# Performance work log

Hardware: AMD Instinct MI355X
Metric: run time of the kernel (lower is better)

The kernel has to match this reference:

```python
import jax, jax.numpy as jnp
import numpy as np

B, S, E, H = 2, 2048, 1024, 16
HD = E // H
SCALE = 1.0 / np.sqrt(HD)
PR_QKV = 0.05   # precision_ratio for q/k/v (critical_attention=False)
PR_OUT = 0.10
ROUTE_THR = 0.05  # gradient_threshold (critical_attention=False)
LN_EPS = 1e-5


def rpb_linear(x, W, b, precision_ratio):
    """ResidualPrecisionBoostLinear: ternary-quantized weight (threshold 0.7*mean|W|,
    per-tensor scale) plus top-`precision_ratio` fraction of residual kept full precision."""
    absW = jnp.abs(W)
    thr = 0.7 * jnp.mean(absW)
    tmask = (absW > thr).astype(W.dtype)
    scale = jnp.sum(absW * tmask) / jnp.maximum(jnp.sum(tmask), 1.0)
    Wq = scale * jnp.sign(W) * tmask
    res = W - Wq
    k = int(precision_ratio * W.size)
    kth = jax.lax.top_k(jnp.abs(res).ravel(), k)[0][-1]
    W_eff = Wq + res * (jnp.abs(res) >= kth).astype(W.dtype)
    return x @ W_eff.T + b


def selective_route(x, threshold):
    # forward: zero out small-magnitude activations (straight-through in training)
    return x * (jnp.abs(x) >= threshold).astype(x.dtype)


def layer_norm(x, g, b):
    mu = jnp.mean(x, axis=-1, keepdims=True)
    var = jnp.mean(jnp.square(x - mu), axis=-1, keepdims=True)
    return (x - mu) * jax.lax.rsqrt(var + LN_EPS) * g + b


def setup_inputs() -> dict:
    key = jax.random.key(0)
    ks = jax.random.split(key, 12)
    f = lambda k, shp, s=1.0: jax.random.normal(k, shp, dtype=jnp.float32) * s
    return {
        "query": f(ks[0], (B, S, E)),
        "key": f(ks[1], (B, S, E)),
        "value": f(ks[2], (B, S, E)),
        "Wq": f(ks[3], (E, E), 0.02), "bq": jnp.zeros((E,), jnp.float32),
        "Wk": f(ks[4], (E, E), 0.02), "bk": jnp.zeros((E,), jnp.float32),
        "Wv": f(ks[5], (E, E), 0.02), "bv": jnp.zeros((E,), jnp.float32),
        "Wo": f(ks[6], (E, E), 0.02), "bo": jnp.zeros((E,), jnp.float32),
        "ln_g": jnp.ones((E,), jnp.float32),
        "ln_b": jnp.zeros((E,), jnp.float32),
    }


def reference(query, key, value, Wq, bq, Wk, bk, Wv, bv, Wo, bo, ln_g, ln_b):
    qn = layer_norm(query, ln_g, ln_b)
    q = selective_route(rpb_linear(qn, Wq, bq, PR_QKV), ROUTE_THR)
    k = selective_route(rpb_linear(key, Wk, bk, PR_QKV), ROUTE_THR)
    v = selective_route(rpb_linear(value, Wv, bv, PR_QKV), ROUTE_THR)
    # [B,S,E] -> [B,H,S,HD]
    q = q.reshape(B, S, H, HD).transpose(0, 2, 1, 3)
    k = k.reshape(B, S, H, HD).transpose(0, 2, 1, 3)
    v = v.reshape(B, S, H, HD).transpose(0, 2, 1, 3)
    scores = jnp.einsum("bhqd,bhkd->bhqk", q, k) * SCALE
    attn = jax.nn.softmax(scores, axis=-1)   # dropout is identity in eval
    ctx = jnp.einsum("bhqk,bhkd->bhqd", attn, v)
    ctx = ctx.transpose(0, 2, 1, 3).reshape(B, S, E)
    return rpb_linear(ctx, Wo, bo, PR_OUT)
```

## Files before the change

kernel.cpp:

```cpp
#include <hip/hip_runtime.h>
#include <stdio.h>
#include <stdint.h>

#define BB 2
#define SS 2048
#define ED 1024
#define HH 16
#define HDD 64
#define MROWS 4096
#define NW_ELEM 1048576u

typedef unsigned short ushortT;
typedef __attribute__((ext_vector_type(8))) short bf16x8;
typedef __attribute__((ext_vector_type(4))) float f32x4;
typedef __attribute__((ext_vector_type(16))) float f32x16;

#define U_WHI 0u
#define U_WLO 4194304u
#define U_XQ  8388608u
#define U_XK  12582912u
#define U_XV  16777216u
#define U_QH  20971520u
#define U_KH  25165824u
#define U_VH  29360128u
#define LP_OFF  33554432u
#define P0_OFF  67108864u
#define P1_OFF  83886080u
#define SMALL_OFF  100663296u
#define HIST_OFF   SMALL_OFF
#define ABS_OFF    (SMALL_OFF + 16384u)
#define MSK_OFF    (ABS_OFF + 32u)
#define CNT_OFF    (MSK_OFF + 32u)
#define SMALL_BYTES 16464u
#define WS_NEEDED  (SMALL_OFF + SMALL_BYTES)

#define SC44 17592186044416.0f
#define INV44 (1.0 / 17592186044416.0)
#define QSCALE 0.18033688011112042f

__device__ __forceinline__ const float* wsel(int w, const float* W0, const float* W1,
                                             const float* W2, const float* W3) {
  return w == 0 ? W0 : w == 1 ? W1 : w == 2 ? W2 : W3;
}

__device__ __forceinline__ ushortT f2bf(float x) {
  unsigned u = __float_as_uint(x);
  unsigned r = (u + 0x7FFFu + ((u >> 16) & 1u)) >> 16;
  return (ushortT)r;
}
__device__ __forceinline__ float bf2f(ushortT b) {
  return __uint_as_float(((unsigned)b) << 16);
}
__device__ __forceinline__ void bsplit(float x, ushortT& h, ushortT& l) {
  ushortT hb = f2bf(x);
  float hf = bf2f(hb);
  h = hb;
  l = f2bf(x - hf);
}
__device__ __forceinline__ unsigned pkbf(float a, float b) {
  unsigned r;
  asm("v_cvt_pk_bf16_f32 %0, %1, %2" : "=v"(r) : "v"(a), "v"(b));
  return r;
}
__device__ __forceinline__ void plswap(unsigned& a, unsigned& b) {
  asm("v_permlane32_swap_b32 %0, %1" : "+v"(a), "+v"(b));
}

__device__ __forceinline__ void gld_lds16(const ushortT* g, ushortT* s) {
  __builtin_amdgcn_global_load_lds((__attribute__((address_space(1))) void*)g,
                                   (__attribute__((address_space(3))) void*)s, 16, 0, 0);
}

__device__ __forceinline__ float get_thr(const unsigned long long* sAbs, int w) {
  return 0.7f * (float)((double)sAbs[w] * INV44 / 1048576.0);
}
__device__ __forceinline__ float get_scale(const unsigned long long* sMsk,
                                           const unsigned* cnt, int w) {
  double s = (double)sMsk[w] * INV44;
  return (float)s / fmaxf((float)cnt[w], 1.0f);
}

__device__ __forceinline__ void scan_sel(const unsigned* hist, unsigned& k, unsigned& prefix,
                                         unsigned* sh, int t) {
  sh[t] = hist[t];
  __syncthreads();
  for (int off = 1; off < 256; off <<= 1) {
    unsigned add = (t + off < 256) ? sh[t + off] : 0u;
    __syncthreads();
    sh[t] += add;
    __syncthreads();
  }
  int sel = __syncthreads_count((int)(sh[t] >= k)) - 1;
  unsigned suf = sh[sel];
  k -= (suf - hist[sel]);
  prefix = (prefix << 8) | (unsigned)sel;
  __syncthreads();
}

__global__ __launch_bounds__(256) void k_wstats(const float* W0, const float* W1,
                                                const float* W2, const float* W3,
                                                unsigned long long* sAbs) {
  const int w = blockIdx.y, t = threadIdx.x;
  const float* W = wsel(w, W0, W1, W2, W3) + blockIdx.x * 4096;
  unsigned long long s = 0;
#pragma unroll
  for (int r = 0; r < 4; r++) {
    float4 v = *(const float4*)(W + (t + 256 * r) * 4);
    s += (unsigned long long)(fabsf(v.x) * SC44);
    s += (unsigned long long)(fabsf(v.y) * SC44);
    s += (unsigned long long)(fabsf(v.z) * SC44);
    s += (unsigned long long)(fabsf(v.w) * SC44);
  }
  __shared__ unsigned long long sd[256];
  sd[t] = s;
  __syncthreads();
  for (int off = 128; off > 0; off >>= 1) {
    if (t < off) sd[t] += sd[t + off];
    __syncthreads();
  }
  if (!t) atomicAdd(&sAbs[w], sd[0]);
}

__global__ __launch_bounds__(256) void k_masked(const float* W0, const float* W1,
                                                const float* W2, const float* W3,
                                                const unsigned long long* sAbs,
                                                unsigned long long* sMsk, unsigned* sCnt) {
  const int w = blockIdx.y, t = threadIdx.x;
  const float thr = get_thr(sAbs, w);
  const float* W = wsel(w, W0, W1, W2, W3) + blockIdx.x * 4096;
  unsigned long long s = 0;
  unsigned c = 0;
#pragma unroll
  for (int r = 0; r < 4; r++) {
    float4 v = *(const float4*)(W + (t + 256 * r) * 4);
    float xs[4] = {v.x, v.y, v.z, v.w};
#pragma unroll
    for (int q = 0; q < 4; q++) {
      float a = fabsf(xs[q]);
      if (a > thr) { s += (unsigned long long)(a * SC44); c++; }
    }
  }
  __shared__ unsigned long long sd[256];
  __shared__ unsigned sc[256];
  sd[t] = s; sc[t] = c;
  __syncthreads();
  for (int off = 128; off > 0; off >>= 1) {
    if (t < off) { sd[t] += sd[t + off]; sc[t] += sc[t + off]; }
    __syncthreads();
  }
  if (!t) { atomicAdd(&sMsk[w], sd[0]); atomicAdd(&sCnt[w], sc[0]); }
}

__global__ __launch_bounds__(256) void k_hist(const float* W0, const float* W1,
                                              const float* W2, const float* W3,
                                              const unsigned long long* sAbs,
                                              const unsigned long long* sMsk,
                                              const unsigned* sCnt,
                                              unsigned* histG, int pass) {
  const int w = blockIdx.y, t = threadIdx.x;
  __shared__ unsigned sh[256];
  __shared__ unsigned h[256];
  const float thr = get_thr(sAbs, w);
  const float scale = get_scale(sMsk, sCnt, w);
  unsigned k = (w == 3) ? 104857u : 52428u, prefix = 0u;
  for (int pp = 0; pp < pass; pp++)
    scan_sel(histG + (pp * 4 + w) * 256, k, prefix, sh, t);

  h[t] = 0;
  __syncthreads();
  const float* W = wsel(w, W0, W1, W2, W3) + blockIdx.x * 4096;
  const int shift1 = 32 - 8 * pass;
  const int shift2 = 24 - 8 * pass;
#pragma unroll
  for (int r = 0; r < 4; r++) {
    float4 v = *(const float4*)(W + (t + 256 * r) * 4);
    float xs[4] = {v.x, v.y, v.z, v.w};
#pragma unroll
    for (int q = 0; q < 4; q++) {
      float x = xs[q];
      float a = fabsf(x);
      float wq = (a > thr) ? copysignf(scale, x) : 0.0f;
      unsigned bits = __float_as_uint(fabsf(x - wq));
      if (pass == 0) {
        atomicAdd(&h[bits >> 24], 1u);
      } else {
        if ((bits >> shift1) == prefix)
          atomicAdd(&h[(bits >> shift2) & 255u], 1u);
      }
    }
  }
  __syncthreads();
  if (h[t]) atomicAdd(&histG[(pass * 4 + w) * 256 + t], h[t]);
}

__global__ __launch_bounds__(256) void k_weff(const float* W0, const float* W1,
                                              const float* W2, const float* W3,
                                              const unsigned long long* sAbs,
                                              const unsigned long long* sMsk,
                                              const unsigned* sCnt,
                                              const unsigned* histG,
                                              ushortT* Whi, ushortT* Wlo) {
  const int w = blockIdx.y, t = threadIdx.x;
  __shared__ unsigned sh[256];
  const float thr = get_thr(sAbs, w);
  const float scale = get_scale(sMsk, sCnt, w);
  unsigned k = (w == 3) ? 104857u : 52428u, kth = 0u;
  for (int pp = 0; pp < 4; pp++)
    scan_sel(histG + (pp * 4 + w) * 256, k, kth, sh, t);

  const unsigned idx = (blockIdx.x * 256 + t) * 4;
  const float* W = wsel(w, W0, W1, W2, W3);
  float4 v = *(const float4*)(W + idx);
  float xs[4] = {v.x, v.y, v.z, v.w};
  ushort4 h4, l4;
#pragma unroll
  for (int c = 0; c < 4; c++) {
    float x = xs[c];
    float a = fabsf(x);
    float wq = (a > thr) ? copysignf(scale, x) : 0.0f;
    float res = x - wq;
    unsigned bits = __float_as_uint(fabsf(res));
    float we = wq + ((bits >= kth) ? res : 0.0f);
    ushortT hh, ll;
    bsplit(we, hh, ll);
    ((ushortT*)&h4)[c] = hh;
    ((ushortT*)&l4)[c] = ll;
  }
  *(ushort4*)&Whi[(size_t)w * NW_ELEM + idx] = h4;
  *(ushort4*)&Wlo[(size_t)w * NW_ELEM + idx] = l4;
}

__global__ __launch_bounds__(256) void k_pre(const float* __restrict__ query,
                                             const float* __restrict__ key,
                                             const float* __restrict__ value,
                                             const float* __restrict__ g,
                                             const float* __restrict__ b,
                                             ushortT* __restrict__ Xq,
                                             ushortT* __restrict__ Xk,
                                             ushortT* __restrict__ Xv) {
  const int t = threadIdx.x;
  if (blockIdx.y == 0) {
    const int row = blockIdx.x;
    __shared__ float red[8];
    float4 v = *(const float4*)&query[(size_t)row * ED + t * 4];
    float s = v.x + v.y + v.z + v.w;
#pragma unroll
    for (int m = 32; m; m >>= 1) s += __shfl_xor(s, m, 64);
    if ((t & 63) == 0) red[t >> 6] = s;
    __syncthreads();
    float mu = (red[0] + red[1] + red[2] + red[3]) * (1.0f / 1024.0f);
    float dx = v.x - mu, dy = v.y - mu, dz = v.z - mu, dw = v.w - mu;
    float s2 = dx * dx + dy * dy + dz * dz + dw * dw;
#pragma unroll
    for (int m = 32; m; m >>= 1) s2 += __shfl_xor(s2, m, 64);
    if ((t & 63) == 0) red[4 + (t >> 6)] = s2;
    __syncthreads();
    float var = (red[4] + red[5] + red[6] + red[7]) * (1.0f / 1024.0f);
    float inv = rsqrtf(var + 1e-5f);
    float4 gg = *(const float4*)&g[t * 4];
    float4 bb = *(const float4*)&b[t * 4];
    float ys[4] = {dx * inv * gg.x + bb.x, dy * inv * gg.y + bb.y,
                   dz * inv * gg.z + bb.z, dw * inv * gg.w + bb.w};
    ushort4 h4;
#pragma unroll
    for (int c = 0; c < 4; c++) ((ushortT*)&h4)[c] = f2bf(ys[c]);
    *(ushort4*)&Xq[(size_t)row * ED + t * 4] = h4;
  } else {
    const float* src = (blockIdx.y == 1) ? key : value;
    ushortT* dst = (blockIdx.y == 1) ? Xk : Xv;
    const int i = (blockIdx.x * 256 + t) * 4;
    float4 v = *(const float4*)&src[i];
    ushort4 h4;
    h4.x = f2bf(v.x); h4.y = f2bf(v.y); h4.z = f2bf(v.z); h4.w = f2bf(v.w);
    *(ushort4*)&dst[i] = h4;
  }
}

__device__ __forceinline__ f32x4 mfma16(bf16x8 a, bf16x8 b, f32x4 c) {
  return __builtin_amdgcn_mfma_f32_16x16x32_bf16(a, b, c, 0, 0, 0);
}

__global__ __launch_bounds__(256, 2) void k_gemm_qkv(
    const ushortT* __restrict__ Xq, const ushortT* __restrict__ Xk,
    const ushortT* __restrict__ Xv,
    const ushortT* __restrict__ Whi, const ushortT* __restrict__ Wlo,
    const float* __restrict__ bq, const float* __restrict__ bk,
    const float* __restrict__ bv,
    ushortT* __restrict__ Qo, ushortT* __restrict__ Ko, ushortT* __restrict__ Vo) {
  __shared__ __align__(16) ushortT sAh[2 * 8192];
  __shared__ __align__(16) ushortT sBh[2 * 4096];
  __shared__ __align__(16) ushortT sBl[2 * 4096];
  const int t = threadIdx.x;
  const int w = t >> 6, l = t & 63;
  const int wr = w >> 1, wc = w & 1;

  const int which = blockIdx.x >> 9;
  const int wid = blockIdx.x & 511;
  int id2 = (wid & 7) * 64 + (wid >> 3);
  const int m0 = (id2 >> 4) * 128, n0 = (id2 & 15) * 64;

  const ushortT* A = which == 0 ? Xq : which == 1 ? Xk : Xv;
  const ushortT* Wh = Whi + (unsigned)which * NW_ELEM;
  const ushortT* Wl = Wlo + 2u * NW_ELEM;
  const float* bias = which == 0 ? bq : which == 1 ? bk : bv;
  const bool wlo = (which == 2);

  const int sr = l >> 3, sg = l & 7;
  const int swz = sg ^ sr;

  auto stage = [&](int kt, int buf) {
#pragma unroll
    for (int s2 = 0; s2 < 4; s2++) {
      int seg = w * 4 + s2;
      size_t gsrc = (size_t)(m0 + seg * 8 + sr) * ED + kt * 64 + swz * 8;
      gld_lds16(A + gsrc, sAh + buf * 8192 + seg * 512);
    }
#pragma unroll
    for (int s2 = 0; s2 < 2; s2++) {
      int seg = w * 2 + s2;
      size_t gsrc = (size_t)(n0 + seg * 8 + sr) * ED + kt * 64 + swz * 8;
      gld_lds16(Wh + gsrc, sBh + buf * 4096 + seg * 512);
      if (wlo) gld_lds16(Wl + gsrc, sBl + buf * 4096 + seg * 512);
    }
  };

  f32x4 acc[4][2];
#pragma unroll
  for (int i = 0; i < 4; i++)
#pragma unroll
    for (int j = 0; j < 2; j++) acc[i][j] = (f32x4){0.0f, 0.0f, 0.0f, 0.0f};

  auto compute = [&](int buf) {
#pragma unroll
    for (int ks = 0; ks < 2; ks++) {
      bf16x8 ah[4], bh2[2], bl2[2];
      const int G = ks * 4 + (l >> 4);
#pragma unroll
      for (int i = 0; i < 4; i++) {
        int r = wr * 64 + i * 16 + (l & 15);
        ah[i] = *(const bf16x8*)&sAh[buf * 8192 + r * 64 + ((G ^ (l & 7)) << 3)];
      }
#pragma unroll
      for (int j = 0; j < 2; j++) {
        int r = wc * 32 + j * 16 + (l & 15);
        int off = buf * 4096 + r * 64 + ((G ^ (l & 7)) << 3);
        bh2[j] = *(const bf16x8*)&sBh[off];
        if (wlo) bl2[j] = *(const bf16x8*)&sBl[off];
      }
#pragma unroll
      for (int i = 0; i < 4; i++)
#pragma unroll
        for (int j = 0; j < 2; j++) {
          acc[i][j] = mfma16(ah[i], bh2[j], acc[i][j]);
          if (wlo) acc[i][j] = mfma16(ah[i], bl2[j], acc[i][j]);
        }
    }
  };

  stage(0, 0);
  __syncthreads();
  for (int kt = 0; kt < 16; ++kt) {
    if (kt < 15) stage(kt + 1, (kt + 1) & 1);
    compute(kt & 1);
    __syncthreads();
  }

  const int coln = l & 15, row4 = (l >> 4) * 4;
  float bn[2];
#pragma unroll
  for (int j = 0; j < 2; j++) bn[j] = bias[n0 + wc * 32 + j * 16 + coln];
  const int b_ = m0 >> 11, h_ = n0 >> 6;

  if (which < 2) {
    const float osc = (which == 0) ? QSCALE : 1.0f;
    ushortT* C = (which == 0) ? Qo : Ko;
#pragma unroll
    for (int i = 0; i < 4; i++)
#pragma unroll
      for (int j = 0; j < 2; j++) {
        int hd = wc * 32 + j * 16 + coln;
#pragma unroll
        for (int r = 0; r < 4; r++) {
          int m = m0 + wr * 64 + i * 16 + row4 + r;
          int s_ = m & 2047;
          float y = acc[i][j][r] + bn[j];
          y = (fabsf(y) >= 0.05f) ? y : 0.0f;
          y *= osc;
          C[((size_t)(b_ * HH + h_) * SS + s_) * HDD + hd] = f2bf(y);
        }
      }
  } else {
#pragma unroll
    for (int i = 0; i < 4; i++)
#pragma unroll
      for (int j = 0; j < 2; j++) {
        int hd = wc * 32 + j * 16 + coln;
        int s0_ = (m0 + wr * 64 + i * 16 + row4) & 2047;
        ushort4 h4;
#pragma unroll
        for (int r = 0; r < 4; r++) {
          float y = acc[i][j][r] + bn[j];
          y = (fabsf(y) >= 0.05f) ? y : 0.0f;
          ((ushortT*)&h4)[r] = f2bf(y);
        }
        *(ushort4*)&Vo[((size_t)(b_ * HH + h_) * HDD + hd) * SS + s0_] = h4;
      }
  }
}

__global__ __launch_bounds__(256, 2) void k_gemmo(
    const ushortT* __restrict__ Ah, const ushortT* __restrict__ Al,
    const ushortT* __restrict__ Wh, const ushortT* __restrict__ Wl,
    const float* __restrict__ bias, float* __restrict__ Cf) {
  __shared__ __align__(16) ushortT sAh[2 * 4096], sAl[2 * 4096];
  __shared__ __align__(16) ushortT sBh[2 * 2048], sBl[2 * 2048];
  const int t = threadIdx.x;
  const int w = t >> 6, l = t & 63;
  const int wr = w >> 1, wc = w & 1;

  int id = blockIdx.x;
  int id2 = (id & 7) * 64 + (id >> 3);
  const int m0 = (id2 >> 4) * 128, n0 = (id2 & 15) * 64;

  const int srow = l >> 2;
  const int sgr = (l & 3) ^ ((l >> 3) & 3);

  auto stage = [&](int kt, int buf) {
    const int c0 = kt * 32 + sgr * 8;
#pragma unroll
    for (int s2 = 0; s2 < 2; s2++) {
      int seg = w * 2 + s2;
      size_t ga = (size_t)(m0 + seg * 16 + srow) * ED + c0;
      gld_lds16(Ah + ga, sAh + buf * 4096 + seg * 512);
      gld_lds16(Al + ga, sAl + buf * 4096 + seg * 512);
    }
    {
      size_t gb = (size_t)(n0 + w * 16 + srow) * ED + c0;
      gld_lds16(Wh + gb, sBh + buf * 2048 + w * 512);
      gld_lds16(Wl + gb, sBl + buf * 2048 + w * 512);
    }
  };

  f32x4 acc[4][2];
#pragma unroll
  for (int i = 0; i < 4; i++)
#pragma unroll
    for (int j = 0; j < 2; j++) acc[i][j] = (f32x4){0.0f, 0.0f, 0.0f, 0.0f};

  auto compute = [&](int buf) {
    bf16x8 ah[4], al[4], bh2[2], bl2[2];
    const int G = l >> 4;
#pragma unroll
    for (int i = 0; i < 4; i++) {
      int r = wr * 64 + i * 16 + (l & 15);
      int off = buf * 4096 + r * 32 + ((G ^ ((r >> 1) & 3)) << 3);
      ah[i] = *(const bf16x8*)&sAh[off];
      al[i] = *(const bf16x8*)&sAl[off];
    }
#pragma unroll
    for (int j = 0; j < 2; j++) {
      int r = wc * 32 + j * 16 + (l & 15);
      int off = buf * 2048 + r * 32 + ((G ^ ((r >> 1) & 3)) << 3);
      bh2[j] = *(const bf16x8*)&sBh[off];
      bl2[j] = *(const bf16x8*)&sBl[off];
    }
#pragma unroll
    for (int i = 0; i < 4; i++)
#pragma unroll
      for (int j = 0; j < 2; j++) {
        acc[i][j] = mfma16(ah[i], bh2[j], acc[i][j]);
        acc[i][j] = mfma16(ah[i], bl2[j], acc[i][j]);
        acc[i][j] = mfma16(al[i], bh2[j], acc[i][j]);
      }
  };

  stage(0, 0);
  __syncthreads();
  for (int kt = 0; kt < 32; ++kt) {
    if (kt < 31) stage(kt + 1, (kt + 1) & 1);
    compute(kt & 1);
    __syncthreads();
  }

  const int coln = l & 15, row4 = (l >> 4) * 4;
  float bn[2];
#pragma unroll
  for (int j = 0; j < 2; j++) bn[j] = bias[n0 + wc * 32 + j * 16 + coln];
#pragma unroll
  for (int i = 0; i < 4; i++)
#pragma unroll
    for (int j = 0; j < 2; j++) {
      int n = n0 + wc * 32 + j * 16 + coln;
#pragma unroll
      for (int r = 0; r < 4; r++) {
        int m = m0 + wr * 64 + i * 16 + row4 + r;
        Cf[(size_t)m * ED + n] = acc[i][j][r] + bn[j];
      }
    }
}

__device__ __forceinline__ f32x16 mfma32(bf16x8 a, bf16x8 b, f32x16 c) {
  return __builtin_amdgcn_mfma_f32_32x32x16_bf16(a, b, c, 0, 0, 0);
}

__device__ __forceinline__ void exppack(const f32x16& A, float& lsum,
                                        bf16x8& paA, bf16x8& paB) {
  float p[16];
#pragma unroll
  for (int r = 0; r < 16; r++) {
    p[r] = exp2f(A[r]);
    lsum += p[r];
  }
  unsigned c0 = pkbf(p[0], p[1]), c1 = pkbf(p[2], p[3]);
  unsigned c2 = pkbf(p[4], p[5]), c3 = pkbf(p[6], p[7]);
  unsigned c4 = pkbf(p[8], p[9]), c5 = pkbf(p[10], p[11]);
  unsigned c6 = pkbf(p[12], p[13]), c7 = pkbf(p[14], p[15]);
  plswap(c0, c2); plswap(c1, c3); plswap(c4, c6); plswap(c5, c7);
  uint4 ta = make_uint4(c0, c1, c2, c3);
  uint4 tb = make_uint4(c4, c5, c6, c7);
  paA = __builtin_bit_cast(bf16x8, ta);
  paB = __builtin_bit_cast(bf16x8, tb);
}

__global__ __launch_bounds__(256, 4) void k_attn(
    const ushortT* __restrict__ Qh, const ushortT* __restrict__ Kh,
    const ushortT* __restrict__ Vh,
    float* __restrict__ Pp, float* __restrict__ Lp) {
  __shared__ __align__(16) ushortT sK[2 * 4096];
  __shared__ __align__(16) ushortT sV[2 * 4096];

  const int t = threadIdx.x;
  const int w = t >> 6, l = t & 63;
  const int l32 = l & 31, g = l >> 5;

  int id = blockIdx.x;
  int id2 = (id & 7) * 128 + (id >> 3);
  const int bh = id2 >> 5;
  const int qt = (id2 >> 1) & 15;
  const int half = id2 & 1;

  const size_t kqbase = (size_t)bh * (SS * HDD);
  const size_t vbase = (size_t)bh * (HDD * SS);
  const int q0 = qt * 128 + w * 32;
  const int sbase = half * 1024;

  bf16x8 qh[4];
  const size_t qrow = kqbase + (size_t)(q0 + l32) * HDD;
#pragma unroll
  for (int ks = 0; ks < 4; ks++) qh[ks] = *(const bf16x8*)&Qh[qrow + ks * 16 + g * 8];

  f32x16 octx0, octx1;
#pragma unroll
  for (int i = 0; i < 16; i++) { octx0[i] = 0.0f; octx1[i] = 0.0f; }
  float lsum = 0.0f;

  const int srow = l >> 3;
  const int sgr = (l & 7) ^ srow;

  auto stageA = [&](int kt, int buf) {
    const int s0 = sbase + kt * 64;
#pragma unroll
    for (int s2 = 0; s2 < 2; s2++) {
      int seg = w * 2 + s2;
      int row = seg * 8 + srow;
      gld_lds16(Kh + kqbase + (size_t)(s0 + row) * HDD + sgr * 8, sK + buf * 4096 + seg * 512);
      gld_lds16(Vh + vbase + (size_t)row * SS + s0 + sgr * 8, sV + buf * 4096 + seg * 512);
    }
  };

  stageA(0, 0);
  __syncthreads();

  for (int kt = 0; kt < 16; ++kt) {
    if (kt < 15) stageA(kt + 1, (kt + 1) & 1);
    const ushortT* cK = sK + (kt & 1) * 4096;
    const ushortT* cV = sV + (kt & 1) * 4096;

    f32x16 acc0, acc1;
#pragma unroll
    for (int i = 0; i < 16; i++) { acc0[i] = 0.0f; acc1[i] = 0.0f; }
#pragma unroll
    for (int ks = 0; ks < 4; ks++) {
      int sw = ((ks * 2 + g) ^ (l32 & 7)) << 3;
      bf16x8 kh0 = *(const bf16x8*)&cK[l32 * 64 + sw];
      bf16x8 kh1 = *(const bf16x8*)&cK[(32 + l32) * 64 + sw];
      acc0 = mfma32(kh0, qh[ks], acc0);
      acc1 = mfma32(kh1, qh[ks], acc1);
    }

    bf16x8 pa0, pa1, pa2, pa3;
    exppack(acc0, lsum, pa0, pa1);
    exppack(acc1, lsum, pa2, pa3);

#pragma unroll
    for (int js = 0; js < 4; js++) {
      bf16x8 pj = js == 0 ? pa0 : js == 1 ? pa1 : js == 2 ? pa2 : pa3;
      int vsw = ((js * 2 + g) ^ (l32 & 7)) << 3;
      bf16x8 vh0 = *(const bf16x8*)&cV[l32 * 64 + vsw];
      bf16x8 vh1 = *(const bf16x8*)&cV[(32 + l32) * 64 + vsw];
      octx0 = mfma32(pj, vh0, octx0);
      octx1 = mfma32(pj, vh1, octx1);
    }
    __syncthreads();
  }

  float ls = lsum + __shfl_xor(lsum, 32, 64);
  if (g == 0) Lp[half * 65536 + bh * 2048 + q0 + l32] = ls;

  float* P = Pp + (size_t)half * 4194304u;
#pragma unroll
  for (int r = 0; r < 16; r++) {
    int q = (r & 3) + 8 * (r >> 2) + 4 * g;
    size_t pb = ((size_t)bh * 2048 + q0 + q) * 64;
    P[pb + l32] = octx0[r];
    P[pb + 32 + l32] = octx1[r];
  }
}

__global__ __launch_bounds__(256) void k_reduce(const float* __restrict__ Pp,
                                                const float* __restrict__ Lp,
                                                ushortT* __restrict__ ctxH,
                                                ushortT* __restrict__ ctxL) {
  const unsigned i = blockIdx.x * 256 + threadIdx.x;
  const int d = i & 63;
  const int sq = (i >> 6) & 2047;
  const int bh = i >> 17;
  float ls = Lp[bh * 2048 + sq] + Lp[65536 + bh * 2048 + sq];
  float o = (Pp[i] + Pp[4194304u + i]) / ls;
  ushortT hh, ll;
  bsplit(o, hh, ll);
  size_t ci = ((size_t)((bh >> 4) * 2048 + sq)) * 1024 + (bh & 15) * 64 + d;
  ctxH[ci] = hh;
  ctxL[ci] = ll;
}

extern "C" void kernel_launch(void* const* d_in, const int* in_sizes, int n_in,
                              void* d_out, int out_size, void* d_ws, size_t ws_size,
                              hipStream_t stream) {
  const float* query = (const float*)d_in[0];
  const float* key   = (const float*)d_in[1];
  const float* value = (const float*)d_in[2];
  const float* Wq = (const float*)d_in[3];
  const float* bq = (const float*)d_in[4];
  const float* Wk = (const float*)d_in[5];
  const float* bk = (const float*)d_in[6];
  const float* Wv = (const float*)d_in[7];
  const float* bv = (const float*)d_in[8];
  const float* Wo = (const float*)d_in[9];
  const float* bo = (const float*)d_in[10];
  const float* lng = (const float*)d_in[11];
  const float* lnb = (const float*)d_in[12];
  float* out = (float*)d_out;

  if (ws_size < (size_t)WS_NEEDED) {
    fprintf(stderr, "kernel_launch: ws too small (%zu < %u)\n", ws_size, WS_NEEDED);
    return;
  }

  ushortT* wsu = (ushortT*)d_ws;
  ushortT* Whi = wsu + U_WHI;
  ushortT* Wlo = wsu + U_WLO;
  ushortT* Xq  = wsu + U_XQ;
  ushortT* Xk  = wsu + U_XK;
  ushortT* Xv  = wsu + U_XV;
  ushortT* Qhp = wsu + U_QH;
  ushortT* Khp = wsu + U_KH;
  ushortT* Vhp = wsu + U_VH;
  ushortT* Chp = wsu + U_XQ;
  ushortT* Clp = wsu + U_XK;

  char* wsb = (char*)d_ws;
  float* Pp = (float*)(wsb + P0_OFF);
  float* Lp = (float*)(wsb + LP_OFF);
  unsigned* histG = (unsigned*)(wsb + HIST_OFF);
  unsigned long long* sAbs = (unsigned long long*)(wsb + ABS_OFF);
  unsigned long long* sMsk = (unsigned long long*)(wsb + MSK_OFF);
  unsigned* sCnt = (unsigned*)(wsb + CNT_OFF);

  hipMemsetAsync(histG, 0, SMALL_BYTES, stream);

  k_pre<<<dim3(MROWS, 3), 256, 0, stream>>>(query, key, value, lng, lnb, Xq, Xk, Xv);

  dim3 gW(256, 4);
  k_wstats<<<gW, 256, 0, stream>>>(Wq, Wk, Wv, Wo, sAbs);
  k_masked<<<gW, 256, 0, stream>>>(Wq, Wk, Wv, Wo, sAbs, sMsk, sCnt);
  for (int pass = 0; pass < 4; ++pass)
    k_hist<<<gW, 256, 0, stream>>>(Wq, Wk, Wv, Wo, sAbs, sMsk, sCnt, histG, pass);
  k_weff<<<dim3(1024, 4), 256, 0, stream>>>(Wq, Wk, Wv, Wo, sAbs, sMsk, sCnt, histG,
                                            Whi, Wlo);

  k_gemm_qkv<<<1536, 256, 0, stream>>>(Xq, Xk, Xv, Whi, Wlo, bq, bk, bv,
                                       Qhp, Khp, Vhp);

  k_attn<<<1024, 256, 0, stream>>>(Qhp, Khp, Vhp, Pp, Lp);
  k_reduce<<<16384, 256, 0, stream>>>(Pp, Lp, Chp, Clp);

  k_gemmo<<<512, 256, 0, stream>>>(Chp, Clp, Whi + 3 * NW_ELEM, Wlo + 3 * NW_ELEM,
                                   bo, out);
}
```

Baseline: 268.0 us.

## Triple-buffer GEMM and attention pipelines, split V GEMM, vectorize reduce

Merges the QKV and output GEMMs into one templated kernel. It uses three LDS buffers with explicit vmcnt waits and one barrier per K-step, where before it double-buffered and synced twice. The V projection, which needs hi/lo weights, becomes its own launch with BK=32 and higher occupancy, so Q/K blocks no longer carry the extra branch. The attention kernel gets the same 3-stage pipeline and s_setprio around its MFMA sections, with occupancy lowered from 4 to 3 to fit the LDS. The reduce kernel now handles four elements per thread with vector loads and stores. The extra LDS can lower occupancy, and the hand-counted vmcnt values must match the number of loads in flight.

```diff
diff --git a/kernel.cpp b/kernel.cpp
--- a/kernel.cpp
+++ b/kernel.cpp
@@ -71,6 +71,16 @@
                                    (__attribute__((address_space(3))) void*)s, 16, 0, 0);
 }
 
+template <int N> __device__ __forceinline__ void waitv() {
+  if constexpr (N == 0) asm volatile("s_waitcnt vmcnt(0)" ::: "memory");
+  else if constexpr (N == 4) asm volatile("s_waitcnt vmcnt(4)" ::: "memory");
+  else if constexpr (N == 6) asm volatile("s_waitcnt vmcnt(6)" ::: "memory");
+}
+__device__ __forceinline__ void pipe_barrier() {
+  __builtin_amdgcn_s_barrier();
+  __builtin_amdgcn_sched_barrier(0);
+}
+
 __device__ __forceinline__ float get_thr(const unsigned long long* sAbs, int w) {
   return 0.7f * (float)((double)sAbs[w] * INV44 / 1048576.0);
 }
@@ -280,47 +290,69 @@
   return __builtin_amdgcn_mfma_f32_16x16x32_bf16(a, b, c, 0, 0, 0);
 }
 
-__global__ __launch_bounds__(256, 2) void k_gemm_qkv(
-    const ushortT* __restrict__ Xq, const ushortT* __restrict__ Xk,
-    const ushortT* __restrict__ Xv,
-    const ushortT* __restrict__ Whi, const ushortT* __restrict__ Wlo,
-    const float* __restrict__ bq, const float* __restrict__ bk,
-    const float* __restrict__ bv,
-    ushortT* __restrict__ Qo, ushortT* __restrict__ Ko, ushortT* __restrict__ Vo) {
-  __shared__ __align__(16) ushortT sAh[2 * 8192];
-  __shared__ __align__(16) ushortT sBh[2 * 4096];
-  __shared__ __align__(16) ushortT sBl[2 * 4096];
+template <int MODE, bool ALO, bool WLO, int BK, int MINW>
+__global__ __launch_bounds__(256, MINW) void k_gemmP(
+    const ushortT* __restrict__ A0, const ushortT* __restrict__ A0l,
+    const ushortT* __restrict__ A1,
+    const ushortT* __restrict__ Wh, const ushortT* __restrict__ Wl,
+    const float* __restrict__ bias0, const float* __restrict__ bias1,
+    ushortT* __restrict__ Cb0, ushortT* __restrict__ Cb1,
+    float* __restrict__ Cf) {
+  constexpr int ABUF = (BK == 64) ? 8192 : 4096;
+  constexpr int BBUF = (BK == 64) ? 4096 : 2048;
+  constexpr int L = ((BK == 64) ? 4 : 2) * (1 + (ALO ? 1 : 0)) +
+                    ((BK == 64) ? 2 : 1) * (1 + (WLO ? 1 : 0));
+  constexpr int NT = 1024 / BK;
+  __shared__ __align__(16) ushortT sAh[3 * ABUF];
+  __shared__ __align__(16) ushortT sAl[ALO ? 3 * ABUF : 8];
+  __shared__ __align__(16) ushortT sBh[3 * BBUF];
+  __shared__ __align__(16) ushortT sBl[WLO ? 3 * BBUF : 8];
+
   const int t = threadIdx.x;
   const int w = t >> 6, l = t & 63;
   const int wr = w >> 1, wc = w & 1;
 
-  const int which = blockIdx.x >> 9;
+  const int which = (MODE == 0) ? (blockIdx.x >> 9) : 0;
   const int wid = blockIdx.x & 511;
   int id2 = (wid & 7) * 64 + (wid >> 3);
   const int m0 = (id2 >> 4) * 128, n0 = (id2 & 15) * 64;
 
-  const ushortT* A = which == 0 ? Xq : which == 1 ? Xk : Xv;
-  const ushortT* Wh = Whi + (unsigned)which * NW_ELEM;
-  const ushortT* Wl = Wlo + 2u * NW_ELEM;
-  const float* bias = which == 0 ? bq : which == 1 ? bk : bv;
-  const bool wlo = (which == 2);
-
-  const int sr = l >> 3, sg = l & 7;
-  const int swz = sg ^ sr;
+  const ushortT* A = (MODE == 0 && which) ? A1 : A0;
+  const ushortT* Wha = Wh + (MODE == 0 ? (unsigned)which * NW_ELEM : 0u);
+  const float* bias = (MODE == 0 && which) ? bias1 : bias0;
+
+  const int sr = l >> 3, swz = (l & 7) ^ sr;
+  const int srow = l >> 2, sgr = (l & 3) ^ ((l >> 3) & 3);
 
   auto stage = [&](int kt, int buf) {
-#pragma unroll
-    for (int s2 = 0; s2 < 4; s2++) {
-      int seg = w * 4 + s2;
-      size_t gsrc = (size_t)(m0 + seg * 8 + sr) * ED + kt * 64 + swz * 8;
-      gld_lds16(A + gsrc, sAh + buf * 8192 + seg * 512);
-    }
-#pragma unroll
-    for (int s2 = 0; s2 < 2; s2++) {
-      int seg = w * 2 + s2;
-      size_t gsrc = (size_t)(n0 + seg * 8 + sr) * ED + kt * 64 + swz * 8;
-      gld_lds16(Wh + gsrc, sBh + buf * 4096 + seg * 512);
-      if (wlo) gld_lds16(Wl + gsrc, sBl + buf * 4096 + seg * 512);
+    if constexpr (BK == 64) {
+#pragma unroll
+      for (int s2 = 0; s2 < 4; s2++) {
+        int seg = w * 4 + s2;
+        size_t ga = (size_t)(m0 + seg * 8 + sr) * ED + kt * 64 + swz * 8;
+        gld_lds16(A + ga, sAh + buf * ABUF + seg * 512);
+        if constexpr (ALO) gld_lds16(A0l + ga, sAl + buf * ABUF + seg * 512);
+      }
+#pragma unroll
+      for (int s2 = 0; s2 < 2; s2++) {
+        int seg = w * 2 + s2;
+        size_t gb = (size_t)(n0 + seg * 8 + sr) * ED + kt * 64 + swz * 8;
+        gld_lds16(Wha + gb, sBh + buf * BBUF + seg * 512);
+        if constexpr (WLO) gld_lds16(Wl + gb, sBl + buf * BBUF + seg * 512);
+      }
+    } else {
+#pragma unroll
+      for (int s2 = 0; s2 < 2; s2++) {
+        int seg = w * 2 + s2;
+        size_t ga = (size_t)(m0 + seg * 16 + srow) * ED + kt * 32 + sgr * 8;
+        gld_lds16(A + ga, sAh + buf * ABUF + seg * 512);
+        if constexpr (ALO) gld_lds16(A0l + ga, sAl + buf * ABUF + seg * 512);
+      }
+      {
+        size_t gb = (size_t)(n0 + w * 16 + srow) * ED + kt * 32 + sgr * 8;
+        gld_lds16(Wha + gb, sBh + buf * BBUF + w * 512);
+        if constexpr (WLO) gld_lds16(Wl + gb, sBl + buf * BBUF + w * 512);
+      }
     }
   };
 
@@ -331,38 +363,71 @@
     for (int j = 0; j < 2; j++) acc[i][j] = (f32x4){0.0f, 0.0f, 0.0f, 0.0f};
 
   auto compute = [&](int buf) {
-#pragma unroll
-    for (int ks = 0; ks < 2; ks++) {
-      bf16x8 ah[4], bh2[2], bl2[2];
-      const int G = ks * 4 + (l >> 4);
+    if constexpr (BK == 64) {
+#pragma unroll
+      for (int ks = 0; ks < 2; ks++) {
+        bf16x8 ah[4], al[4], bh2[2], bl2[2];
+        const int G = ks * 4 + (l >> 4);
+#pragma unroll
+        for (int i = 0; i < 4; i++) {
+          int r = wr * 64 + i * 16 + (l & 15);
+          int off = buf * ABUF + r * 64 + ((G ^ (l & 7)) << 3);
+          ah[i] = *(const bf16x8*)&sAh[off];
+          if constexpr (ALO) al[i] = *(const bf16x8*)&sAl[off];
+        }
+#pragma unroll
+        for (int j = 0; j < 2; j++) {
+          int r = wc * 32 + j * 16 + (l & 15);
+          int off = buf * BBUF + r * 64 + ((G ^ (l & 7)) << 3);
+          bh2[j] = *(const bf16x8*)&sBh[off];
+          if constexpr (WLO) bl2[j] = *(const bf16x8*)&sBl[off];
+        }
+#pragma unroll
+        for (int i = 0; i < 4; i++)
+#pragma unroll
+          for (int j = 0; j < 2; j++) {
+            acc[i][j] = mfma16(ah[i], bh2[j], acc[i][j]);
+            if constexpr (WLO) acc[i][j] = mfma16(ah[i], bl2[j], acc[i][j]);
+            if constexpr (ALO) acc[i][j] = mfma16(al[i], bh2[j], acc[i][j]);
+          }
+      }
+    } else {
+      bf16x8 ah[4], al[4], bh2[2], bl2[2];
+      const int G = l >> 4;
 #pragma unroll
       for (int i = 0; i < 4; i++) {
         int r = wr * 64 + i * 16 + (l & 15);
-        ah[i] = *(const bf16x8*)&sAh[buf * 8192 + r * 64 + ((G ^ (l & 7)) << 3)];
+        int off = buf * ABUF + r * 32 + ((G ^ ((r >> 1) & 3)) << 3);
+        ah[i] = *(const bf16x8*)&sAh[off];
+        if constexpr (ALO) al[i] = *(const bf16x8*)&sAl[off];
       }
 #pragma unroll
       for (int j = 0; j < 2; j++) {
         int r = wc * 32 + j * 16 + (l & 15);
-        int off = buf * 4096 + r * 64 + ((G ^ (l & 7)) << 3);
+        int off = buf * BBUF + r * 32 + ((G ^ ((r >> 1) & 3)) << 3);
         bh2[j] = *(const bf16x8*)&sBh[off];
-        if (wlo) bl2[j] = *(const bf16x8*)&sBl[off];
+        if constexpr (WLO) bl2[j] = *(const bf16x8*)&sBl[off];
       }
 #pragma unroll
       for (int i = 0; i < 4; i++)
 #pragma unroll
         for (int j = 0; j < 2; j++) {
           acc[i][j] = mfma16(ah[i], bh2[j], acc[i][j]);
-          if (wlo) acc[i][j] = mfma16(ah[i], bl2[j], acc[i][j]);
+          if constexpr (WLO) acc[i][j] = mfma16(ah[i], bl2[j], acc[i][j]);
+          if constexpr (ALO) acc[i][j] = mfma16(al[i], bh2[j], acc[i][j]);
         }
     }
   };
 
   stage(0, 0);
-  __syncthreads();
-  for (int kt = 0; kt < 16; ++kt) {
-    if (kt < 15) stage(kt + 1, (kt + 1) & 1);
-    compute(kt & 1);
-    __syncthreads();
+  stage(1, 1);
+  for (int kt = 0; kt < NT; ++kt) {
+    if (kt < NT - 1) waitv<L>(); else waitv<0>();
+    pipe_barrier();
+    if (kt + 2 < NT) stage(kt + 2, (kt + 2) % 3);
+    __builtin_amdgcn_s_setprio(1);
+    compute(kt % 3);
+    __builtin_amdgcn_s_setprio(0);
   }
 
   const int coln = l & 15, row4 = (l >> 4) * 4;
@@ -371,9 +436,21 @@
   for (int j = 0; j < 2; j++) bn[j] = bias[n0 + wc * 32 + j * 16 + coln];
   const int b_ = m0 >> 11, h_ = n0 >> 6;
 
-  if (which < 2) {
+  if constexpr (MODE == 1) {
+#pragma unroll
+    for (int i = 0; i < 4; i++)
+#pragma unroll
+      for (int j = 0; j < 2; j++) {
+        int n = n0 + wc * 32 + j * 16 + coln;
+#pragma unroll
+        for (int r = 0; r < 4; r++) {
+          int m = m0 + wr * 64 + i * 16 + row4 + r;
+          Cf[(size_t)m * ED + n] = acc[i][j][r] + bn[j];
+        }
+      }
+  } else if constexpr (MODE == 0) {
     const float osc = (which == 0) ? QSCALE : 1.0f;
-    ushortT* C = (which == 0) ? Qo : Ko;
+    ushortT* C = which ? Cb1 : Cb0;
 #pragma unroll
     for (int i = 0; i < 4; i++)
 #pragma unroll
@@ -403,100 +480,9 @@
           y = (fabsf(y) >= 0.05f) ? y : 0.0f;
           ((ushortT*)&h4)[r] = f2bf(y);
         }
-        *(ushort4*)&Vo[((size_t)(b_ * HH + h_) * HDD + hd) * SS + s0_] = h4;
-      }
-  }
-}
-
-__global__ __launch_bounds__(256, 2) void k_gemmo(
-    const ushortT* __restrict__ Ah, const ushortT* __restrict__ Al,
-    const ushortT* __restrict__ Wh, const ushortT* __restrict__ Wl,
-    const float* __restrict__ bias, float* __restrict__ Cf) {
-  __shared__ __align__(16) ushortT sAh[2 * 4096], sAl[2 * 4096];
-  __shared__ __align__(16) ushortT sBh[2 * 2048], sBl[2 * 2048];
-  const int t = threadIdx.x;
-  const int w = t >> 6, l = t & 63;
-  const int wr = w >> 1, wc = w & 1;
-
-  int id = blockIdx.x;
-  int id2 = (id & 7) * 64 + (id >> 3);
-  const int m0 = (id2 >> 4) * 128, n0 = (id2 & 15) * 64;
-
-  const int srow = l >> 2;
-  const int sgr = (l & 3) ^ ((l >> 3) & 3);
-
-  auto stage = [&](int kt, int buf) {
-    const int c0 = kt * 32 + sgr * 8;
-#pragma unroll
-    for (int s2 = 0; s2 < 2; s2++) {
-      int seg = w * 2 + s2;
-      size_t ga = (size_t)(m0 + seg * 16 + srow) * ED + c0;
-      gld_lds16(Ah + ga, sAh + buf * 4096 + seg * 512);
-      gld_lds16(Al + ga, sAl + buf * 4096 + seg * 512);
-    }
-    {
-      size_t gb = (size_t)(n0 + w * 16 + srow) * ED + c0;
-      gld_lds16(Wh + gb, sBh + buf * 2048 + w * 512);
-      gld_lds16(Wl + gb, sBl + buf * 2048 + w * 512);
-    }
-  };
-
-  f32x4 acc[4][2];
-#pragma unroll
-  for (int i = 0; i < 4; i++)
-#pragma unroll
-    for (int j = 0; j < 2; j++) acc[i][j] = (f32x4){0.0f, 0.0f, 0.0f, 0.0f};
-
-  auto compute = [&](int buf) {
-    bf16x8 ah[4], al[4], bh2[2], bl2[2];
-    const int G = l >> 4;
-#pragma unroll
-    for (int i = 0; i < 4; i++) {
-      int r = wr * 64 + i * 16 + (l & 15);
-      int off = buf * 4096 + r * 32 + ((G ^ ((r >> 1) & 3)) << 3);
-      ah[i] = *(const bf16x8*)&sAh[off];
-      al[i] = *(const bf16x8*)&sAl[off];
-    }
-#pragma unroll
-    for (int j = 0; j < 2; j++) {
-      int r = wc * 32 + j * 16 + (l & 15);
-      int off = buf * 2048 + r * 32 + ((G ^ ((r >> 1) & 3)) << 3);
-      bh2[j] = *(const bf16x8*)&sBh[off];
-      bl2[j] = *(const bf16x8*)&sBl[off];
-    }
-#pragma unroll
-    for (int i = 0; i < 4; i++)
-#pragma unroll
-      for (int j = 0; j < 2; j++) {
-        acc[i][j] = mfma16(ah[i], bh2[j], acc[i][j]);
-        acc[i][j] = mfma16(ah[i], bl2[j], acc[i][j]);
-        acc[i][j] = mfma16(al[i], bh2[j], acc[i][j]);
-      }
-  };
-
-  stage(0, 0);
-  __syncthreads();
-  for (int kt = 0; kt < 32; ++kt) {
-    if (kt < 31) stage(kt + 1, (kt + 1) & 1);
-    compute(kt & 1);
-    __syncthreads();
-  }
-
-  const int coln = l & 15, row4 = (l >> 4) * 4;
-  float bn[2];
-#pragma unroll
-  for (int j = 0; j < 2; j++) bn[j] = bias[n0 + wc * 32 + j * 16 + coln];
-#pragma unroll
-  for (int i = 0; i < 4; i++)
-#pragma unroll
-    for (int j = 0; j < 2; j++) {
-      int n = n0 + wc * 32 + j * 16 + coln;
-#pragma unroll
-      for (int r = 0; r < 4; r++) {
-        int m = m0 + wr * 64 + i * 16 + row4 + r;
-        Cf[(size_t)m * ED + n] = acc[i][j][r] + bn[j];
-      }
-    }
+        *(ushort4*)&Cb0[((size_t)(b_ * HH + h_) * HDD + hd) * SS + s0_] = h4;
+      }
+  }
 }
 
 __device__ __forceinline__ f32x16 mfma32(bf16x8 a, bf16x8 b, f32x16 c) {
@@ -522,12 +508,12 @@
   paB = __builtin_bit_cast(bf16x8, tb);
 }
 
-__global__ __launch_bounds__(256, 4) void k_attn(
+__global__ __launch_bounds__(256, 3) void k_attn(
     const ushortT* __restrict__ Qh, const ushortT* __restrict__ Kh,
     const ushortT* __restrict__ Vh,
     float* __restrict__ Pp, float* __restrict__ Lp) {
-  __shared__ __align__(16) ushortT sK[2 * 4096];
-  __shared__ __align__(16) ushortT sV[2 * 4096];
+  __shared__ __align__(16) ushortT sK[3 * 4096];
+  __shared__ __align__(16) ushortT sV[3 * 4096];
 
   const int t = threadIdx.x;
   const int w = t >> 6, l = t & 63;
@@ -569,16 +555,19 @@
   };
 
   stageA(0, 0);
-  __syncthreads();
+  stageA(1, 1);
 
   for (int kt = 0; kt < 16; ++kt) {
-    if (kt < 15) stageA(kt + 1, (kt + 1) & 1);
-    const ushortT* cK = sK + (kt & 1) * 4096;
-    const ushortT* cV = sV + (kt & 1) * 4096;
+    if (kt < 15) waitv<4>(); else waitv<0>();
+    pipe_barrier();
+    if (kt + 2 < 16) stageA(kt + 2, (kt + 2) % 3);
+    const ushortT* cK = sK + (kt % 3) * 4096;
+    const ushortT* cV = sV + (kt % 3) * 4096;
 
     f32x16 acc0, acc1;
 #pragma unroll
     for (int i = 0; i < 16; i++) { acc0[i] = 0.0f; acc1[i] = 0.0f; }
+    __builtin_amdgcn_s_setprio(1);
 #pragma unroll
     for (int ks = 0; ks < 4; ks++) {
       int sw = ((ks * 2 + g) ^ (l32 & 7)) << 3;
@@ -587,11 +576,13 @@
       acc0 = mfma32(kh0, qh[ks], acc0);
       acc1 = mfma32(kh1, qh[ks], acc1);
     }
+    __builtin_amdgcn_s_setprio(0);
 
     bf16x8 pa0, pa1, pa2, pa3;
     exppack(acc0, lsum, pa0, pa1);
     exppack(acc1, lsum, pa2, pa3);
 
+    __builtin_amdgcn_s_setprio(1);
 #pragma unroll
     for (int js = 0; js < 4; js++) {
       bf16x8 pj = js == 0 ? pa0 : js == 1 ? pa1 : js == 2 ? pa2 : pa3;
@@ -601,7 +592,7 @@
       octx0 = mfma32(pj, vh0, octx0);
       octx1 = mfma32(pj, vh1, octx1);
     }
-    __syncthreads();
+    __builtin_amdgcn_s_setprio(0);
   }
 
   float ls = lsum + __shfl_xor(lsum, 32, 64);
@@ -621,17 +612,27 @@
                                                 const float* __restrict__ Lp,
                                                 ushortT* __restrict__ ctxH,
                                                 ushortT* __restrict__ ctxL) {
-  const unsigned i = blockIdx.x * 256 + threadIdx.x;
-  const int d = i & 63;
-  const int sq = (i >> 6) & 2047;
-  const int bh = i >> 17;
+  const unsigned i4 = (blockIdx.x * 256 + threadIdx.x) * 4;
+  const int d = i4 & 63;
+  const int sq = (i4 >> 6) & 2047;
+  const int bh = i4 >> 17;
   float ls = Lp[bh * 2048 + sq] + Lp[65536 + bh * 2048 + sq];
-  float o = (Pp[i] + Pp[4194304u + i]) / ls;
-  ushortT hh, ll;
-  bsplit(o, hh, ll);
+  float inv = 1.0f / ls;
+  float4 a = *(const float4*)&Pp[i4];
+  float4 b = *(const float4*)&Pp[4194304u + i4];
+  float os[4] = {(a.x + b.x) * inv, (a.y + b.y) * inv,
+                 (a.z + b.z) * inv, (a.w + b.w) * inv};
+  ushort4 h4, l4;
+#pragma unroll
+  for (int c = 0; c < 4; c++) {
+    ushortT hh, ll;
+    bsplit(os[c], hh, ll);
+    ((ushortT*)&h4)[c] = hh;
+    ((ushortT*)&l4)[c] = ll;
+  }
   size_t ci = ((size_t)((bh >> 4) * 2048 + sq)) * 1024 + (bh & 15) * 64 + d;
-  ctxH[ci] = hh;
-  ctxL[ci] = ll;
+  *(ushort4*)&ctxH[ci] = h4;
+  *(ushort4*)&ctxL[ci] = l4;
 }
 
 extern "C" void kernel_launch(void* const* d_in, const int* in_sizes, int n_in,
@@ -689,12 +690,16 @@
   k_weff<<<dim3(1024, 4), 256, 0, stream>>>(Wq, Wk, Wv, Wo, sAbs, sMsk, sCnt, histG,
                                             Whi, Wlo);
 
-  k_gemm_qkv<<<1536, 256, 0, stream>>>(Xq, Xk, Xv, Whi, Wlo, bq, bk, bv,
-                                       Qhp, Khp, Vhp);
+  k_gemmP<0, false, false, 64, 2><<<1024, 256, 0, stream>>>(
+      Xq, nullptr, Xk, Whi, nullptr, bq, bk, Qhp, Khp, nullptr);
+  k_gemmP<2, false, true, 32, 3><<<512, 256, 0, stream>>>(
+      Xv, nullptr, nullptr, Whi + 2 * NW_ELEM, Wlo + 2 * NW_ELEM, bv, nullptr,
+      Vhp, nullptr, nullptr);
 
   k_attn<<<1024, 256, 0, stream>>>(Qhp, Khp, Vhp, Pp, Lp);
-  k_reduce<<<16384, 256, 0, stream>>>(Pp, Lp, Chp, Clp);
-
-  k_gemmo<<<512, 256, 0, stream>>>(Chp, Clp, Whi + 3 * NW_ELEM, Wlo + 3 * NW_ELEM,
-                                   bo, out);
-}
+  k_reduce<<<4096, 256, 0, stream>>>(Pp, Lp, Chp, Clp);
+
+  k_gemmP<1, true, true, 32, 2><<<512, 256, 0, stream>>>(
+      Chp, Clp, nullptr, Whi + 3 * NW_ELEM, Wlo + 3 * NW_ELEM, bo, nullptr,
+      nullptr, nullptr, out);
+}
```

After: 258.3 us. 3.6% less time.
